# Kernel optimization log

Measured on AMD Instinct MI355X. Metric: run time of the kernel, lower is better.

The kernel has to match this reference:

```python
import jax, jax.numpy as jnp
import numpy as np

B, H, K, NUM_PTR, MAX_LEN = 32768, 896, 2000, 2, 128


def setup_inputs() -> dict:
    key = jax.random.key(0)
    k1, k2, k3 = jax.random.split(key, 3)
    z = jax.random.normal(k1, (B, H), dtype=jnp.float32)
    # codebook init: normal(0, 0.02) as in torch.nn.init.normal_
    emb = 0.02 * jax.random.normal(k2, (K, H), dtype=jnp.float32)
    # pointer heads: two Linear(H, MAX_LEN) layers, stacked
    W = jax.random.normal(k3, (NUM_PTR, MAX_LEN, H), dtype=jnp.float32) / np.float32(np.sqrt(H))
    b = jnp.zeros((NUM_PTR, MAX_LEN), dtype=jnp.float32)
    return {"z": z, "emb": emb, "W": W, "b": b, "prompt_len": 96}


def reference(z, emb, W, b, prompt_len):
    # --- quantize: L2 cdist + argmin + gather + straight-through ---
    # dist[b,k] = ||z_b||^2 - 2 z_b . e_k + ||e_k||^2   -> [B, K]
    dist = (jnp.sum(z * z, axis=1, keepdims=True)
            - 2.0 * (z @ emb.T)
            + jnp.sum(emb * emb, axis=1)[None, :])
    idx = jnp.argmin(dist, axis=1)            # [B]
    z_q = emb[idx]                            # [B, H]
    op_state = z + jax.lax.stop_gradient(z_q - z)
    # --- pointer heads with prompt-length mask ---
    logits = jnp.einsum('bh,plh->bpl', z, W) + b[None, :, :]   # [B, 2, MAX_LEN]
    mask = jnp.where(jnp.arange(logits.shape[-1]) < prompt_len, 0.0, -jnp.inf)
    ptr_logits = logits + mask[None, None, :]
    return op_state, ptr_logits
```

## Files before the change

kernel.cpp:

```cpp
#include <hip/hip_runtime.h>
#include <hip/hip_bf16.h>
#include <cstdint>
#include <cstddef>

#define B_SZ 32768
#define H_SZ 896
#define K_SZ 2000
#define KPAD 2048
#define NPTR_COLS 256
#define NCAT 2304
#define BM 128
#define BN 128
#define BK 32

typedef float floatx4 __attribute__((ext_vector_type(4)));
typedef __bf16 bf16x8 __attribute__((ext_vector_type(8)));

#define MASK_NEG 1.0e30f

__device__ inline unsigned short f2bf_rne(float x) {
  unsigned u = __builtin_bit_cast(unsigned, x);
  unsigned r = u + 0x7fffu + ((u >> 16) & 1u);
  return (unsigned short)(r >> 16);
}
__device__ inline float bf2f(unsigned short b) {
  unsigned u = ((unsigned)b) << 16;
  return __builtin_bit_cast(float, u);
}

typedef __attribute__((address_space(1))) void GV;
typedef __attribute__((address_space(3))) void LV;
__device__ inline void load_lds16(const void* gsrc, void* ldst) {
  __builtin_amdgcn_global_load_lds((GV*)gsrc, (LV*)ldst, 16, 0, 0);
}

__global__ __launch_bounds__(256) void convert_kernel(
    const float* __restrict__ emb, const float* __restrict__ W,
    unsigned short* __restrict__ cat_hi, unsigned short* __restrict__ cat_lo,
    float* __restrict__ normE) {
  const int row = blockIdx.x;
  const int tid = threadIdx.x;
  const float* src = nullptr;
  bool zero = false;
  if (row < K_SZ)       src = emb + (size_t)row * H_SZ;
  else if (row < KPAD)  zero = true;
  else                  src = W + (size_t)(row - KPAD) * H_SZ;

  float ss = 0.f;
  for (int c = tid; c < H_SZ; c += 256) {
    float x = zero ? 0.f : src[c];
    unsigned short hb = f2bf_rne(x);
    float hf = bf2f(hb);
    unsigned short lb = f2bf_rne(x - hf);
    cat_hi[(size_t)row * H_SZ + c] = hb;
    cat_lo[(size_t)row * H_SZ + c] = lb;
    ss += x * x;
  }
  #pragma unroll
  for (int off = 32; off > 0; off >>= 1) ss += __shfl_down(ss, off);
  __shared__ float wsum[4];
  const int wave = tid >> 6, lane = tid & 63;
  if (lane == 0) wsum[wave] = ss;
  __syncthreads();
  if (tid == 0 && row < KPAD) normE[row] = wsum[0] + wsum[1] + wsum[2] + wsum[3];
}

__global__ __launch_bounds__(256, 2) void main_gemm(
    const float* __restrict__ z,
    const unsigned short* __restrict__ cat_hi,
    const unsigned short* __restrict__ cat_lo,
    const float* __restrict__ normE,
    const float* __restrict__ bias,
    const int* __restrict__ plen_p,
    float* __restrict__ pmin, int* __restrict__ pidx,
    float* __restrict__ out_logits) {
  __shared__ unsigned short Ahi[BM * BK], Alo[BM * BK];
  __shared__ unsigned short Bhi[BN * BK], Blo[BN * BK];
  __shared__ float red_v[2][BM];
  __shared__ int   red_i[2][BM];

  const int tid = threadIdx.x;
  const int wave = tid >> 6, lane = tid & 63;
  const int wm = wave >> 1, wn = wave & 1;
  const int bx = blockIdx.x, split = blockIdx.y;
  const int b0 = bx * BM;
  const int lrow = lane & 15, lk = lane >> 4;

  float minv[16];
  int   mini[16];
  #pragma unroll
  for (int s = 0; s < 16; ++s) { minv[s] = 3.4e38f; mini[s] = 0; }

  const int t0 = split * 8;
  const int tcount = (split == 2) ? 2 : 8;

  const int arow = tid >> 1, ahalf = tid & 1;
  const float* zsrc = z + (size_t)(b0 + arow) * H_SZ + ahalf * 16;
  unsigned short* a_hi_dst = &Ahi[arow * BK + ahalf * 16];
  unsigned short* a_lo_dst = &Alo[arow * BK + ahalf * 16];

  for (int tt = t0; tt < t0 + tcount; ++tt) {
    const int n0 = tt * BN;
    floatx4 acc[4][4];
    #pragma unroll
    for (int i = 0; i < 4; ++i)
      #pragma unroll
      for (int j = 0; j < 4; ++j) acc[i][j] = (floatx4){0.f, 0.f, 0.f, 0.f};

    for (int kk = 0; kk < H_SZ; kk += BK) {
      float xv[16];
      #pragma unroll
      for (int q = 0; q < 4; ++q) {
        const float4 f = *(const float4*)(zsrc + kk + q * 4);
        xv[q * 4 + 0] = f.x; xv[q * 4 + 1] = f.y;
        xv[q * 4 + 2] = f.z; xv[q * 4 + 3] = f.w;
      }
      unsigned hv[8], lv[8];
      #pragma unroll
      for (int q = 0; q < 8; ++q) {
        unsigned short h0 = f2bf_rne(xv[2 * q]), h1 = f2bf_rne(xv[2 * q + 1]);
        float r0 = xv[2 * q] - bf2f(h0), r1 = xv[2 * q + 1] - bf2f(h1);
        unsigned short l0 = f2bf_rne(r0), l1 = f2bf_rne(r1);
        hv[q] = (unsigned)h0 | ((unsigned)h1 << 16);
        lv[q] = (unsigned)l0 | ((unsigned)l1 << 16);
      }
      *(uint4*)(a_hi_dst)     = make_uint4(hv[0], hv[1], hv[2], hv[3]);
      *(uint4*)(a_hi_dst + 8) = make_uint4(hv[4], hv[5], hv[6], hv[7]);
      *(uint4*)(a_lo_dst)     = make_uint4(lv[0], lv[1], lv[2], lv[3]);
      *(uint4*)(a_lo_dst + 8) = make_uint4(lv[4], lv[5], lv[6], lv[7]);

      #pragma unroll
      for (int s = 0; s < 2; ++s) {
        const int seg = wave * 2 + s;
        const int nrow = n0 + seg * 16 + (lane >> 2);
        const size_t goff = (size_t)nrow * H_SZ + kk + (lane & 3) * 8;
        load_lds16(cat_hi + goff, &Bhi[seg * 16 * BK]);
        load_lds16(cat_lo + goff, &Blo[seg * 16 * BK]);
      }
      __syncthreads();

      bf16x8 ah[4], al[4], bh[4], bl[4];
      #pragma unroll
      for (int i = 0; i < 4; ++i) {
        const int r = (wm * 64 + i * 16 + lrow) * BK + lk * 8;
        ah[i] = *(const bf16x8*)&Ahi[r];
        al[i] = *(const bf16x8*)&Alo[r];
      }
      #pragma unroll
      for (int j = 0; j < 4; ++j) {
        const int r = (wn * 64 + j * 16 + lrow) * BK + lk * 8;
        bh[j] = *(const bf16x8*)&Bhi[r];
        bl[j] = *(const bf16x8*)&Blo[r];
      }
      #pragma unroll
      for (int i = 0; i < 4; ++i)
        #pragma unroll
        for (int j = 0; j < 4; ++j) {
          acc[i][j] = __builtin_amdgcn_mfma_f32_16x16x32_bf16(ah[i], bh[j], acc[i][j], 0, 0, 0);
          acc[i][j] = __builtin_amdgcn_mfma_f32_16x16x32_bf16(ah[i], bl[j], acc[i][j], 0, 0, 0);
          acc[i][j] = __builtin_amdgcn_mfma_f32_16x16x32_bf16(al[i], bh[j], acc[i][j], 0, 0, 0);
        }
      __syncthreads();
    }

    if (split < 2) {
      #pragma unroll
      for (int j = 0; j < 4; ++j) {
        const int k = n0 + wn * 64 + j * 16 + lrow;
        const float nE = normE[k];
        const bool valid = (k < K_SZ);
        #pragma unroll
        for (int i = 0; i < 4; ++i)
          #pragma unroll
          for (int r = 0; r < 4; ++r) {
            float v = nE - 2.0f * acc[i][j][r];
            if (!valid) v = 3.4e38f;
            const int s = i * 4 + r;
            if (v < minv[s]) { minv[s] = v; mini[s] = k; }
          }
      }
    } else {
      const int plen = *plen_p;
      #pragma unroll
      for (int j = 0; j < 4; ++j) {
        const int c = (n0 - KPAD) + wn * 64 + j * 16 + lrow;
        const float bv = bias[c];
        const bool masked = ((c & 127) >= plen);
        #pragma unroll
        for (int i = 0; i < 4; ++i) {
          const int growbase = b0 + wm * 64 + i * 16 + lk * 4;
          #pragma unroll
          for (int r = 0; r < 4; ++r) {
            const float val = masked ? -MASK_NEG : (acc[i][j][r] + bv);
            out_logits[(size_t)(growbase + r) * NPTR_COLS + c] = val;
          }
        }
      }
    }
  }

  if (split < 2) {
    #pragma unroll
    for (int s = 0; s < 16; ++s) {
      float v = minv[s]; int id = mini[s];
      #pragma unroll
      for (int m = 1; m < 16; m <<= 1) {
        const float ov = __shfl_xor(v, m);
        const int   oid = __shfl_xor(id, m);
        if (ov < v || (ov == v && oid < id)) { v = ov; id = oid; }
      }
      if (lrow == 0) {
        const int row_local = wm * 64 + (s >> 2) * 16 + lk * 4 + (s & 3);
        red_v[wn][row_local] = v;
        red_i[wn][row_local] = id;
      }
    }
    __syncthreads();
    if (tid < BM) {
      const float v0 = red_v[0][tid], v1 = red_v[1][tid];
      float v; int id;
      if (v1 < v0) { v = v1; id = red_i[1][tid]; }
      else         { v = v0; id = red_i[0][tid]; }
      pmin[(size_t)split * B_SZ + b0 + tid] = v;
      pidx[(size_t)split * B_SZ + b0 + tid] = id;
    }
  }
}

__global__ __launch_bounds__(256) void merge_gather(
    const float* __restrict__ z, const float* __restrict__ emb,
    const float* __restrict__ pmin, const int* __restrict__ pidx,
    float* __restrict__ out0) {
  const int row = blockIdx.x;
  const float v0 = pmin[row], v1 = pmin[B_SZ + row];
  const int id = (v1 < v0) ? pidx[B_SZ + row] : pidx[row];
  const float4* e4 = (const float4*)(emb + (size_t)id * H_SZ);
  const float4* z4 = (const float4*)(z + (size_t)row * H_SZ);
  float4* o4 = (float4*)(out0 + (size_t)row * H_SZ);
  const int t = threadIdx.x;
  if (t < H_SZ / 4) {
    const float4 zz = z4[t], ee = e4[t];
    float4 r;
    r.x = zz.x + (ee.x - zz.x);
    r.y = zz.y + (ee.y - zz.y);
    r.z = zz.z + (ee.z - zz.z);
    r.w = zz.w + (ee.w - zz.w);
    o4[t] = r;
  }
}

extern "C" void kernel_launch(void* const* d_in, const int* in_sizes, int n_in,
                              void* d_out, int out_size, void* d_ws, size_t ws_size,
                              hipStream_t stream) {
  const float* z    = (const float*)d_in[0];
  const float* emb  = (const float*)d_in[1];
  const float* W    = (const float*)d_in[2];
  const float* bias = (const float*)d_in[3];
  const int*   plen = (const int*)d_in[4];
  float* out = (float*)d_out;

  char* ws = (char*)d_ws;
  unsigned short* cat_hi = (unsigned short*)(ws);
  unsigned short* cat_lo = (unsigned short*)(ws + 4128768);
  float* normE = (float*)(ws + 8257536);
  float* pmin  = (float*)(ws + 8265728);
  int*   pidx  = (int*)(ws + 8527872);
  float* out_logits = out + (size_t)B_SZ * H_SZ;

  convert_kernel<<<dim3(NCAT), dim3(256), 0, stream>>>(emb, W, cat_hi, cat_lo, normE);
  main_gemm<<<dim3(B_SZ / BM, 3), dim3(256), 0, stream>>>(
      z, cat_hi, cat_lo, normE, bias, plen, pmin, pidx, out_logits);
  merge_gather<<<dim3(B_SZ), dim3(256), 0, stream>>>(z, emb, pmin, pidx, out);
}
```

Measured before the change: 721.4 us.

## Pre-split z into bf16 hi/lo, load A via LDS DMA, balance split tiles

Adds a separate pass that splits z into bf16 hi/lo planes once, stored temporarily in the op_state output buffer. The GEMM then loads A tiles straight into LDS with the async load path instead of converting fp32 in registers on every N tile, and uses an XOR swizzle on LDS reads to avoid bank conflicts. The 18 N tiles are rebalanced to 6 per split, so every split now also computes a partial argmin, and the merge step takes three partials. The cost is an extra kernel plus a write and re-read of the bf16 z planes, and a dependency on the output buffer being overwritten later by merge_gather.

```diff
diff --git a/kernel.cpp b/kernel.cpp
--- a/kernel.cpp
+++ b/kernel.cpp
@@ -12,6 +12,7 @@
 #define BM 128
 #define BN 128
 #define BK 32
+#define TPS 6
 
 typedef float floatx4 __attribute__((ext_vector_type(4)));
 typedef __bf16 bf16x8 __attribute__((ext_vector_type(8)));
@@ -65,8 +66,30 @@
   if (tid == 0 && row < KPAD) normE[row] = wsum[0] + wsum[1] + wsum[2] + wsum[3];
 }
 
+__global__ __launch_bounds__(256) void convert_z(
+    const float* __restrict__ z,
+    unsigned short* __restrict__ zhi, unsigned short* __restrict__ zlo) {
+  const size_t t = (size_t)blockIdx.x * 256 + threadIdx.x;
+  const float* src = z + t * 8;
+  float x[8];
+  *(float4*)&x[0] = *(const float4*)src;
+  *(float4*)&x[4] = *(const float4*)(src + 4);
+  unsigned hv[4], lv[4];
+  #pragma unroll
+  for (int q = 0; q < 4; ++q) {
+    unsigned short h0 = f2bf_rne(x[2 * q]), h1 = f2bf_rne(x[2 * q + 1]);
+    float r0 = x[2 * q] - bf2f(h0), r1 = x[2 * q + 1] - bf2f(h1);
+    unsigned short l0 = f2bf_rne(r0), l1 = f2bf_rne(r1);
+    hv[q] = (unsigned)h0 | ((unsigned)h1 << 16);
+    lv[q] = (unsigned)l0 | ((unsigned)l1 << 16);
+  }
+  *(uint4*)(zhi + t * 8) = make_uint4(hv[0], hv[1], hv[2], hv[3]);
+  *(uint4*)(zlo + t * 8) = make_uint4(lv[0], lv[1], lv[2], lv[3]);
+}
+
 __global__ __launch_bounds__(256, 2) void main_gemm(
-    const float* __restrict__ z,
+    const unsigned short* __restrict__ zhi,
+    const unsigned short* __restrict__ zlo,
     const unsigned short* __restrict__ cat_hi,
     const unsigned short* __restrict__ cat_lo,
     const float* __restrict__ normE,
@@ -85,22 +108,39 @@
   const int bx = blockIdx.x, split = blockIdx.y;
   const int b0 = bx * BM;
   const int lrow = lane & 15, lk = lane >> 4;
+  const int csw = ((lk ^ ((lrow >> 1) & 3)) << 3);
+
+  const int srow = lane >> 2;
+  const int scol = (((lane & 3) ^ ((lane >> 3) & 3)) << 3);
 
   float minv[16];
   int   mini[16];
   #pragma unroll
   for (int s = 0; s < 16; ++s) { minv[s] = 3.4e38f; mini[s] = 0; }
 
-  const int t0 = split * 8;
-  const int tcount = (split == 2) ? 2 : 8;
-
-  const int arow = tid >> 1, ahalf = tid & 1;
-  const float* zsrc = z + (size_t)(b0 + arow) * H_SZ + ahalf * 16;
-  unsigned short* a_hi_dst = &Ahi[arow * BK + ahalf * 16];
-  unsigned short* a_lo_dst = &Alo[arow * BK + ahalf * 16];
-
-  for (int tt = t0; tt < t0 + tcount; ++tt) {
+  const unsigned short* pa_hi[2];
+  const unsigned short* pa_lo[2];
+  #pragma unroll
+  for (int s = 0; s < 2; ++s) {
+    const int seg = wave * 2 + s;
+    const size_t off = (size_t)(b0 + seg * 16 + srow) * H_SZ + scol;
+    pa_hi[s] = zhi + off;
+    pa_lo[s] = zlo + off;
+  }
+
+  const int t0 = split * TPS;
+  for (int tt = t0; tt < t0 + TPS; ++tt) {
     const int n0 = tt * BN;
+    const unsigned short* pb_hi[2];
+    const unsigned short* pb_lo[2];
+    #pragma unroll
+    for (int s = 0; s < 2; ++s) {
+      const int seg = wave * 2 + s;
+      const size_t off = (size_t)(n0 + seg * 16 + srow) * H_SZ + scol;
+      pb_hi[s] = cat_hi + off;
+      pb_lo[s] = cat_lo + off;
+    }
+
     floatx4 acc[4][4];
     #pragma unroll
     for (int i = 0; i < 4; ++i)
@@ -108,47 +148,26 @@
       for (int j = 0; j < 4; ++j) acc[i][j] = (floatx4){0.f, 0.f, 0.f, 0.f};
 
     for (int kk = 0; kk < H_SZ; kk += BK) {
-      float xv[16];
-      #pragma unroll
-      for (int q = 0; q < 4; ++q) {
-        const float4 f = *(const float4*)(zsrc + kk + q * 4);
-        xv[q * 4 + 0] = f.x; xv[q * 4 + 1] = f.y;
-        xv[q * 4 + 2] = f.z; xv[q * 4 + 3] = f.w;
-      }
-      unsigned hv[8], lv[8];
-      #pragma unroll
-      for (int q = 0; q < 8; ++q) {
-        unsigned short h0 = f2bf_rne(xv[2 * q]), h1 = f2bf_rne(xv[2 * q + 1]);
-        float r0 = xv[2 * q] - bf2f(h0), r1 = xv[2 * q + 1] - bf2f(h1);
-        unsigned short l0 = f2bf_rne(r0), l1 = f2bf_rne(r1);
-        hv[q] = (unsigned)h0 | ((unsigned)h1 << 16);
-        lv[q] = (unsigned)l0 | ((unsigned)l1 << 16);
-      }
-      *(uint4*)(a_hi_dst)     = make_uint4(hv[0], hv[1], hv[2], hv[3]);
-      *(uint4*)(a_hi_dst + 8) = make_uint4(hv[4], hv[5], hv[6], hv[7]);
-      *(uint4*)(a_lo_dst)     = make_uint4(lv[0], lv[1], lv[2], lv[3]);
-      *(uint4*)(a_lo_dst + 8) = make_uint4(lv[4], lv[5], lv[6], lv[7]);
-
       #pragma unroll
       for (int s = 0; s < 2; ++s) {
         const int seg = wave * 2 + s;
-        const int nrow = n0 + seg * 16 + (lane >> 2);
-        const size_t goff = (size_t)nrow * H_SZ + kk + (lane & 3) * 8;
-        load_lds16(cat_hi + goff, &Bhi[seg * 16 * BK]);
-        load_lds16(cat_lo + goff, &Blo[seg * 16 * BK]);
+        load_lds16(pa_hi[s] + kk, &Ahi[seg * 512]);
+        load_lds16(pa_lo[s] + kk, &Alo[seg * 512]);
+        load_lds16(pb_hi[s] + kk, &Bhi[seg * 512]);
+        load_lds16(pb_lo[s] + kk, &Blo[seg * 512]);
       }
       __syncthreads();
 
       bf16x8 ah[4], al[4], bh[4], bl[4];
       #pragma unroll
       for (int i = 0; i < 4; ++i) {
-        const int r = (wm * 64 + i * 16 + lrow) * BK + lk * 8;
+        const int r = (wm * 64 + i * 16 + lrow) * BK + csw;
         ah[i] = *(const bf16x8*)&Ahi[r];
         al[i] = *(const bf16x8*)&Alo[r];
       }
       #pragma unroll
       for (int j = 0; j < 4; ++j) {
-        const int r = (wn * 64 + j * 16 + lrow) * BK + lk * 8;
+        const int r = (wn * 64 + j * 16 + lrow) * BK + csw;
         bh[j] = *(const bf16x8*)&Bhi[r];
         bl[j] = *(const bf16x8*)&Blo[r];
       }
@@ -163,7 +182,7 @@
       __syncthreads();
     }
 
-    if (split < 2) {
+    if (tt < 16) {
       #pragma unroll
       for (int j = 0; j < 4; ++j) {
         const int k = n0 + wn * 64 + j * 16 + lrow;
@@ -199,31 +218,29 @@
     }
   }
 
-  if (split < 2) {
+  #pragma unroll
+  for (int s = 0; s < 16; ++s) {
+    float v = minv[s]; int id = mini[s];
     #pragma unroll
-    for (int s = 0; s < 16; ++s) {
-      float v = minv[s]; int id = mini[s];
-      #pragma unroll
-      for (int m = 1; m < 16; m <<= 1) {
-        const float ov = __shfl_xor(v, m);
-        const int   oid = __shfl_xor(id, m);
-        if (ov < v || (ov == v && oid < id)) { v = ov; id = oid; }
-      }
-      if (lrow == 0) {
-        const int row_local = wm * 64 + (s >> 2) * 16 + lk * 4 + (s & 3);
-        red_v[wn][row_local] = v;
-        red_i[wn][row_local] = id;
-      }
-    }
-    __syncthreads();
-    if (tid < BM) {
-      const float v0 = red_v[0][tid], v1 = red_v[1][tid];
-      float v; int id;
-      if (v1 < v0) { v = v1; id = red_i[1][tid]; }
-      else         { v = v0; id = red_i[0][tid]; }
-      pmin[(size_t)split * B_SZ + b0 + tid] = v;
-      pidx[(size_t)split * B_SZ + b0 + tid] = id;
-    }
+    for (int m = 1; m < 16; m <<= 1) {
+      const float ov = __shfl_xor(v, m);
+      const int   oid = __shfl_xor(id, m);
+      if (ov < v || (ov == v && oid < id)) { v = ov; id = oid; }
+    }
+    if (lrow == 0) {
+      const int row_local = wm * 64 + (s >> 2) * 16 + lk * 4 + (s & 3);
+      red_v[wn][row_local] = v;
+      red_i[wn][row_local] = id;
+    }
+  }
+  __syncthreads();
+  if (tid < BM) {
+    const float v0 = red_v[0][tid], v1 = red_v[1][tid];
+    float v; int id;
+    if (v1 < v0) { v = v1; id = red_i[1][tid]; }
+    else         { v = v0; id = red_i[0][tid]; }
+    pmin[(size_t)split * B_SZ + b0 + tid] = v;
+    pidx[(size_t)split * B_SZ + b0 + tid] = id;
   }
 }
 
@@ -232,8 +249,12 @@
     const float* __restrict__ pmin, const int* __restrict__ pidx,
     float* __restrict__ out0) {
   const int row = blockIdx.x;
-  const float v0 = pmin[row], v1 = pmin[B_SZ + row];
-  const int id = (v1 < v0) ? pidx[B_SZ + row] : pidx[row];
+  float v = pmin[row];
+  int  id = pidx[row];
+  const float v1 = pmin[B_SZ + row];
+  if (v1 < v) { v = v1; id = pidx[B_SZ + row]; }
+  const float v2 = pmin[2 * (size_t)B_SZ + row];
+  if (v2 < v) { v = v2; id = pidx[2 * (size_t)B_SZ + row]; }
   const float4* e4 = (const float4*)(emb + (size_t)id * H_SZ);
   const float4* z4 = (const float4*)(z + (size_t)row * H_SZ);
   float4* o4 = (float4*)(out0 + (size_t)row * H_SZ);
@@ -264,11 +285,15 @@
   unsigned short* cat_lo = (unsigned short*)(ws + 4128768);
   float* normE = (float*)(ws + 8257536);
   float* pmin  = (float*)(ws + 8265728);
-  int*   pidx  = (int*)(ws + 8527872);
+  int*   pidx  = (int*)(ws + 8658944);
+
+  unsigned short* zhi = (unsigned short*)out;
+  unsigned short* zlo = zhi + (size_t)B_SZ * H_SZ;
   float* out_logits = out + (size_t)B_SZ * H_SZ;
 
   convert_kernel<<<dim3(NCAT), dim3(256), 0, stream>>>(emb, W, cat_hi, cat_lo, normE);
+  convert_z<<<dim3(B_SZ * H_SZ / (256 * 8)), dim3(256), 0, stream>>>(z, zhi, zlo);
   main_gemm<<<dim3(B_SZ / BM, 3), dim3(256), 0, stream>>>(
-      z, cat_hi, cat_lo, normE, bias, plen, pmin, pidx, out_logits);
+      zhi, zlo, cat_hi, cat_lo, normE, bias, plen, pmin, pidx, out_logits);
   merge_gather<<<dim3(B_SZ), dim3(256), 0, stream>>>(z, emb, pmin, pidx, out);
 }
```

New measurement: 744.8 us. 1.03x slower.
